# Optimization experiments

Measured on AMD Instinct MI355X. Metric: run time of the kernel, lower is better.

The kernel has to match this reference:

```python
import jax, jax.numpy as jnp
import numpy as np

SLOPE = 25.0  # fast-sigmoid surrogate slope (snntorch default)

@jax.custom_vjp
def spike(u):
    # Heaviside spike with fast-sigmoid surrogate gradient
    return (u > 0).astype(u.dtype)

def _spike_fwd(u):
    return spike(u), u

def _spike_bwd(u, g):
    return (g / (1.0 + SLOPE * jnp.abs(u)) ** 2,)

spike.defvjp(_spike_fwd, _spike_bwd)


def setup_inputs() -> dict:
    key = jax.random.key(0)
    B, N_IN, T = 256, 700, 100
    H1, H2, O = 2048, 2048, 20
    ks = jax.random.split(key, 6)

    def lin(k, out_d, in_d):
        s = 1.0 / np.sqrt(in_d)
        kw, kb = jax.random.split(k)
        W = jax.random.uniform(kw, (out_d, in_d), minval=-s, maxval=s, dtype=jnp.float32)
        b = jax.random.uniform(kb, (out_d,), minval=-s, maxval=s, dtype=jnp.float32)
        return W, b

    W1, b1 = lin(ks[0], H1, N_IN)
    W2, b2 = lin(ks[1], H2, H1)
    V, _ = lin(ks[2], H2, H2)  # learned recurrent weight of RecurrentAhpc
    W3, b3 = lin(ks[3], O, H2)
    data = jax.random.normal(ks[4], (B, N_IN, T), dtype=jnp.float32)
    f32 = lambda v: jnp.asarray(v, jnp.float32)
    return dict(
        data=data,
        W1=W1, b1=b1, W2=W2, b2=b2, V=V, W3=W3, b3=b3,
        beta1=f32(0.9), thr1=f32(1.0),
        beta_r=f32(0.9), thr_r=f32(1.0),
        back_beta=f32(0.85), alpha=f32(0.6),
        beta2=f32(0.9), thr2=f32(1.0),
    )


def _forward(data, W1, b1, W2, b2, V, W3, b3,
             beta1, thr1, beta_r, thr_r, back_beta, alpha, beta2, thr2):
    B = data.shape[0]
    H1, H2, O = W1.shape[0], W2.shape[0], W3.shape[0]
    xs = jnp.transpose(data, (2, 0, 1))  # [T, B, N_in]
    z = lambda d: jnp.zeros((B, d), dtype=data.dtype)
    init = (z(H1), z(H2), z(H2), z(H2), z(O))  # mem1, mem_r, ahp, spk_r, mem2

    def step(carry, x_t):
        mem1, mem_r, ahp, spk_r, mem2 = carry
        # layer 1: Linear + Leaky (reset-by-subtract)
        mem1 = beta1 * mem1 + x_t @ W1.T + b1
        s1 = spike(mem1 - thr1)
        mem1 = mem1 - s1 * thr1
        # layer 2: Linear + recurrent AHP leaky neuron
        cur = s1 @ W2.T + b2 + spk_r @ V.T
        mem_r = beta_r * mem_r + cur - ahp
        s_r = spike(mem_r - thr_r)
        mem_r = mem_r - s_r * thr_r
        ahp = back_beta * ahp + alpha * s_r  # after-hyperpolarization current
        # layer 3: Linear + Leaky output
        mem2 = beta2 * mem2 + s_r @ W3.T + b3
        s2 = spike(mem2 - thr2)
        mem2 = mem2 - s2 * thr2
        return (mem1, mem_r, ahp, s_r, mem2), s2

    _, spk_rec = jax.lax.scan(step, init, xs)
    return spk_rec  # [T, B, num_outputs]


def reference(data, W1, b1, W2, b2, V, W3, b3,
              beta1, thr1, beta_r, thr_r, back_beta, alpha, beta2, thr2):
    return _forward(data, W1, b1, W2, b2, V, W3, b3,
                    beta1, thr1, beta_r, thr_r, back_beta, alpha, beta2, thr2)
```

## Files before the change

kernel.cpp:

```cpp
#include <hip/hip_runtime.h>
#include <hip/hip_bf16.h>
#include <cstdint>

#define T_STEPS 100
#define BATCH 256
#define NIN 700
#define H1 2048
#define H2 2048
#define NOUT 20
#define VKS 8
#define TCHUNK 10

typedef __attribute__((ext_vector_type(8))) short bf16x8;
typedef __attribute__((ext_vector_type(4))) float f32x4;
typedef unsigned long long ull;

__device__ __forceinline__ void async16(void* lds, const void* g) {
    __builtin_amdgcn_global_load_lds(
        (const __attribute__((address_space(1))) unsigned int*)g,
        (__attribute__((address_space(3))) unsigned int*)lds, 16, 0, 0);
}

__device__ __forceinline__ unsigned short f2bf(float x) {
    __hip_bfloat16 h = __float2bfloat16(x);
    return *(unsigned short*)&h;
}
__device__ __forceinline__ float bf2f(unsigned short u) {
    __hip_bfloat16 h = *(__hip_bfloat16*)&u;
    return __bfloat162float(h);
}

__global__ __launch_bounds__(256) void split_kernel(
    const float* __restrict__ W2, const float* __restrict__ V,
    unsigned short* __restrict__ Bsplit)
{
    const size_t D = (size_t)2048 * 4096;
    size_t i = (size_t)blockIdx.x * 256 + threadIdx.x;
    int j = (int)(i >> 12), k = (int)(i & 4095);
    float w = (k < 2048) ? W2[(size_t)j * 2048 + k] : V[(size_t)j * 2048 + (k - 2048)];
    unsigned short h = f2bf(w);
    float r1 = w - bf2f(h);
    unsigned short m = f2bf(r1);
    float r2 = r1 - bf2f(m);
    unsigned short l = f2bf(r2);
    Bsplit[i] = h;
    Bsplit[D + i] = m;
    Bsplit[2 * D + i] = l;
}

__global__ __launch_bounds__(256) void w1split_kernel(
    const float* __restrict__ W1, unsigned short* __restrict__ W1f)
{
    const size_t P = (size_t)88 * 2048 * 8;
    int id = blockIdx.x * 256 + threadIdx.x;
    int g = id >> 11, j = id & 2047;
    unsigned short h8[8], m8[8], l8[8];
    #pragma unroll
    for (int e = 0; e < 8; ++e) {
        int k = g * 8 + e;
        float v = (k < NIN) ? W1[(size_t)j * NIN + k] : 0.f;
        unsigned short h = f2bf(v); float r1 = v - bf2f(h);
        unsigned short m = f2bf(r1); float r2 = r1 - bf2f(m);
        h8[e] = h; m8[e] = m; l8[e] = f2bf(r2);
    }
    size_t base = (((size_t)g * 2048) + j) * 8;
    *(uint4*)(W1f + base)         = *(uint4*)h8;
    *(uint4*)(W1f + P + base)     = *(uint4*)m8;
    *(uint4*)(W1f + 2 * P + base) = *(uint4*)l8;
}

__global__ __launch_bounds__(256) void l1m_kernel(
    const float* __restrict__ data, const unsigned short* __restrict__ W1f,
    const float* __restrict__ b1,
    const float* __restrict__ p_beta1, const float* __restrict__ p_thr1,
    ull* __restrict__ s1bits)
{
    __shared__ __align__(16) char smem[33280];
    unsigned short* Af = (unsigned short*)smem;
    const int tid = threadIdx.x, lane = tid & 63, w = tid >> 6;
    const int n16 = lane & 15, q = lane >> 4;
    const int jt = blockIdx.x & 7, b = blockIdx.x >> 3;
    const int j0w = jt * 256 + w * 64;
    const float* xb = data + (size_t)b * (NIN * T_STEPS);
    const size_t P = (size_t)88 * 2048 * 8;

    f32x4 acc[7][4] = {};
    for (int c = 0; c < 22; ++c) {
        const int kbase = c * 32;
        for (int it = tid; it < 448; it += 256) {
            int g = it / 112, t = it - g * 112;
            unsigned short h8[8], m8[8], l8[8];
            #pragma unroll
            for (int e = 0; e < 8; ++e) {
                int k = kbase + g * 8 + e;
                float v = (t < T_STEPS && k < NIN) ? xb[(size_t)k * T_STEPS + t] : 0.f;
                unsigned short h = f2bf(v); float r1 = v - bf2f(h);
                unsigned short m = f2bf(r1); float r2 = r1 - bf2f(m);
                h8[e] = h; m8[e] = m; l8[e] = f2bf(r2);
            }
            unsigned short* dst = Af + g * 896 + t * 8;
            *(uint4*)(dst)        = *(uint4*)h8;
            *(uint4*)(dst + 3584) = *(uint4*)m8;
            *(uint4*)(dst + 7168) = *(uint4*)l8;
        }
        __syncthreads();
        bf16x8 bh[4], bm[4], bl[4];
        const size_t gq = (size_t)(c * 4 + q);
        #pragma unroll
        for (int n = 0; n < 4; ++n) {
            size_t off = (gq * 2048 + (size_t)(j0w + n * 16 + n16)) * 8;
            bh[n] = *(const bf16x8*)(W1f + off);
            bm[n] = *(const bf16x8*)(W1f + P + off);
            bl[n] = *(const bf16x8*)(W1f + 2 * P + off);
        }
        #pragma unroll
        for (int m = 0; m < 7; ++m) {
            const unsigned short* ap = Af + q * 896 + (m * 16 + n16) * 8;
            bf16x8 ah = *(const bf16x8*)(ap);
            bf16x8 am = *(const bf16x8*)(ap + 3584);
            bf16x8 al = *(const bf16x8*)(ap + 7168);
            #pragma unroll
            for (int n = 0; n < 4; ++n) {
                acc[m][n] = __builtin_amdgcn_mfma_f32_16x16x32_bf16(ah, bh[n], acc[m][n], 0, 0, 0);
                acc[m][n] = __builtin_amdgcn_mfma_f32_16x16x32_bf16(ah, bm[n], acc[m][n], 0, 0, 0);
                acc[m][n] = __builtin_amdgcn_mfma_f32_16x16x32_bf16(am, bh[n], acc[m][n], 0, 0, 0);
                acc[m][n] = __builtin_amdgcn_mfma_f32_16x16x32_bf16(ah, bl[n], acc[m][n], 0, 0, 0);
                acc[m][n] = __builtin_amdgcn_mfma_f32_16x16x32_bf16(al, bh[n], acc[m][n], 0, 0, 0);
                acc[m][n] = __builtin_amdgcn_mfma_f32_16x16x32_bf16(am, bm[n], acc[m][n], 0, 0, 0);
            }
        }
        __syncthreads();
    }
    float* Cw = (float*)smem + w * (32 * 65);
    const float beta1 = *p_beta1, thr1 = *p_thr1;
    const float b1j = b1[j0w + lane];
    float mem = 0.f;
    for (int s = 0; s < 4; ++s) {
        #pragma unroll
        for (int mm = 0; mm < 2; ++mm) {
            int m = s * 2 + mm;
            if (m < 7) {
                #pragma unroll
                for (int n = 0; n < 4; ++n)
                    #pragma unroll
                    for (int r = 0; r < 4; ++r)
                        Cw[(mm * 16 + q * 4 + r) * 65 + n * 16 + n16] = acc[m][n][r];
            }
        }
        int tcnt = (s < 3) ? 32 : 4;
        for (int tt = 0; tt < tcnt; ++tt) {
            float v = Cw[tt * 65 + lane];
            mem = fmaf(beta1, mem, v) + b1j;
            bool pred = (mem - thr1) > 0.f;
            ull mask = __ballot(pred);
            if (pred) mem -= thr1;
            if (lane == 0) {
                int tg = s * 32 + tt;
                s1bits[((size_t)tg * BATCH + b) * 32 + jt * 4 + w] = mask;
            }
        }
    }
}

__global__ __launch_bounds__(256) void expand_kernel(
    const ull* __restrict__ bits_t0,
    unsigned short* __restrict__ plane)
{
    const int row = blockIdx.x;
    const int tid = threadIdx.x;
    ull word = bits_t0[(size_t)row * 32 + (tid >> 3)];
    unsigned int byte = (unsigned int)(word >> ((tid & 7) * 8)) & 0xFFu;
    unsigned short o8[8];
    #pragma unroll
    for (int e = 0; e < 8; ++e)
        o8[e] = (byte >> e) & 1u ? (unsigned short)0x3F80 : (unsigned short)0;
    *(uint4*)(plane + (size_t)row * 2048 + tid * 8) = *(uint4*)o8;
}

__global__ __launch_bounds__(256, 2) void xw2_kernel(
    const unsigned short* __restrict__ S1c,
    const unsigned short* __restrict__ Bsplit,
    float* __restrict__ X2c)
{
    __shared__ __align__(16) unsigned short Alds[128 * 64];
    __shared__ __align__(16) unsigned short Blds[3 * 64 * 64];
    const int bid = blockIdx.x;
    const int x = bid & 7;
    const int i = bid >> 3;
    const int ntl = i / 20;
    const int mt = i - ntl * 20;
    const int n0 = (x * 4 + ntl) << 6;
    const int tid = threadIdx.x, lane = tid & 63, w = tid >> 6;
    const unsigned short* Abase = S1c + ((size_t)mt << 7) * 2048;
    f32x4 acc[2][4] = {};
    for (int c = 0; c < 32; ++c) {
        const int kin = c << 6;
        #pragma unroll
        for (int ii = 0; ii < 4; ++ii) {
            int gi = (ii << 8) + tid;
            int row = gi >> 3, g8 = gi & 7;
            async16(Alds + ((size_t)gi << 3),
                    Abase + (size_t)row * 2048 + kin + ((g8 ^ (row & 7)) << 3));
        }
        #pragma unroll
        for (int term = 0; term < 3; ++term) {
            const unsigned short* Bg = Bsplit + ((size_t)term << 23);
            #pragma unroll
            for (int ii = 0; ii < 2; ++ii) {
                int d = (w << 7) + (ii << 6) + lane;
                int row = d >> 3, g8 = d & 7;
                async16(Blds + (((term << 9) + (w << 7) + (ii << 6)) << 3),
                        Bg + (size_t)(n0 + row) * 4096 + kin + ((g8 ^ (row & 7)) << 3));
            }
        }
        __syncthreads();
        #pragma unroll
        for (int kk = 0; kk < 2; ++kk) {
            const int q = lane >> 4, k16 = (kk << 2) + q;
            bf16x8 af[2];
            #pragma unroll
            for (int ii = 0; ii < 2; ++ii) {
                int ra = (w << 5) + (ii << 4) + (lane & 15);
                af[ii] = *(const bf16x8*)(Alds + (((ra << 3) + (k16 ^ (ra & 7))) << 3));
            }
            #pragma unroll
            for (int term = 0; term < 3; ++term) {
                bf16x8 bfr[4];
                #pragma unroll
                for (int j = 0; j < 4; ++j) {
                    int rb = (j << 4) + (lane & 15);
                    bfr[j] = *(const bf16x8*)(Blds +
                              (((term << 9) + (rb << 3) + (k16 ^ (rb & 7))) << 3));
                }
                #pragma unroll
                for (int ii = 0; ii < 2; ++ii)
                    #pragma unroll
                    for (int j = 0; j < 4; ++j)
                        acc[ii][j] = __builtin_amdgcn_mfma_f32_16x16x32_bf16(
                            af[ii], bfr[j], acc[ii][j], 0, 0, 0);
            }
        }
        __syncthreads();
    }
    float* Xp = X2c + ((size_t)mt << 7) * 2048;
    #pragma unroll
    for (int ii = 0; ii < 2; ++ii) {
        int rg = (w << 5) + (ii << 4) + ((lane >> 4) << 2);
        #pragma unroll
        for (int j = 0; j < 4; ++j) {
            int cg = n0 + (j << 4) + (lane & 15);
            #pragma unroll
            for (int r = 0; r < 4; ++r)
                Xp[(size_t)(rg + r) * 2048 + cg] = acc[ii][j][r];
        }
    }
}

__global__ __launch_bounds__(256, 2) void vgemm_kernel(
    const unsigned short* __restrict__ spk,
    const unsigned short* __restrict__ Bsplit,
    float* __restrict__ Cpart)
{
    __shared__ __align__(16) unsigned short Alds[256 * 64];
    __shared__ __align__(16) unsigned short Blds[3 * 64 * 64];
    const int bid = blockIdx.x;
    const int nt = bid & 31, ks = bid >> 5;
    const int n0 = nt << 6;
    const int tid = threadIdx.x, lane = tid & 63, w = tid >> 6;
    f32x4 acc[4][4] = {};
    for (int c = 0; c < 4; ++c) {
        const int kin = (ks << 8) + (c << 6);
        #pragma unroll
        for (int ii = 0; ii < 8; ++ii) {
            int gi = (ii << 8) + tid;
            int row = gi >> 3, g8 = gi & 7;
            async16(Alds + ((size_t)gi << 3),
                    spk + (size_t)row * 2048 + kin + ((g8 ^ (row & 7)) << 3));
        }
        #pragma unroll
        for (int term = 0; term < 3; ++term) {
            const unsigned short* Bg = Bsplit + ((size_t)term << 23);
            #pragma unroll
            for (int ii = 0; ii < 2; ++ii) {
                int d = (w << 7) + (ii << 6) + lane;
                int row = d >> 3, g8 = d & 7;
                async16(Blds + (((term << 9) + (w << 7) + (ii << 6)) << 3),
                        Bg + (size_t)(n0 + row) * 4096 + 2048 + kin + ((g8 ^ (row & 7)) << 3));
            }
        }
        __syncthreads();
        #pragma unroll
        for (int kk = 0; kk < 2; ++kk) {
            const int q = lane >> 4, k16 = (kk << 2) + q;
            bf16x8 af[4];
            #pragma unroll
            for (int ii = 0; ii < 4; ++ii) {
                int ra = (w << 6) + (ii << 4) + (lane & 15);
                af[ii] = *(const bf16x8*)(Alds + (((ra << 3) + (k16 ^ (ra & 7))) << 3));
            }
            #pragma unroll
            for (int term = 0; term < 3; ++term) {
                bf16x8 bfr[4];
                #pragma unroll
                for (int j = 0; j < 4; ++j) {
                    int rb = (j << 4) + (lane & 15);
                    bfr[j] = *(const bf16x8*)(Blds +
                              (((term << 9) + (rb << 3) + (k16 ^ (rb & 7))) << 3));
                }
                #pragma unroll
                for (int ii = 0; ii < 4; ++ii)
                    #pragma unroll
                    for (int j = 0; j < 4; ++j)
                        acc[ii][j] = __builtin_amdgcn_mfma_f32_16x16x32_bf16(
                            af[ii], bfr[j], acc[ii][j], 0, 0, 0);
            }
        }
        __syncthreads();
    }
    float* Cp = Cpart + ((size_t)ks << 19);
    #pragma unroll
    for (int ii = 0; ii < 4; ++ii) {
        int rg = (w << 6) + (ii << 4) + ((lane >> 4) << 2);
        #pragma unroll
        for (int j = 0; j < 4; ++j) {
            int cg = n0 + (j << 4) + (lane & 15);
            #pragma unroll
            for (int r = 0; r < 4; ++r)
                Cp[(size_t)(rg + r) * 2048 + cg] = acc[ii][j][r];
        }
    }
}

__global__ __launch_bounds__(256) void l2fin_kernel(
    const float* __restrict__ Cpart, const float* __restrict__ X2t,
    const float* __restrict__ b2,
    float* __restrict__ mem_r, float* __restrict__ ahp,
    unsigned short* __restrict__ spk_out,
    ull* __restrict__ srbits_t,
    const float* __restrict__ p_beta_r, const float* __restrict__ p_thr_r,
    const float* __restrict__ p_back_beta, const float* __restrict__ p_alpha)
{
    const int b = blockIdx.x, t = threadIdx.x;
    const int lane = t & 63, wv = t >> 6;
    const float beta_r = *p_beta_r, thr_r = *p_thr_r;
    const float bb = *p_back_beta, al = *p_alpha;
    #pragma unroll
    for (int u = 0; u < 8; ++u) {
        int j = t + (u << 8);
        size_t cidx = (size_t)b * 2048 + j;
        float x = 0.f;
        #pragma unroll
        for (int p = 0; p < VKS; ++p) x += Cpart[((size_t)p << 19) + cidx];
        float cur = x + X2t[cidx] + b2[j];
        float m = fmaf(beta_r, mem_r[cidx], cur) - ahp[cidx];
        bool pred = (m - thr_r) > 0.f;
        ull mask = __ballot(pred);
        float s = pred ? 1.f : 0.f;
        if (pred) m -= thr_r;
        mem_r[cidx] = m;
        ahp[cidx] = fmaf(bb, ahp[cidx], al * s);
        spk_out[cidx] = pred ? (unsigned short)0x3F80 : (unsigned short)0;
        if (lane == 0) srbits_t[((size_t)b << 5) + (u << 2) + wv] = mask;
    }
}

__global__ __launch_bounds__(256) void w3out_kernel(
    const ull* __restrict__ srbits, const float* __restrict__ W3,
    const float* __restrict__ b3, float* __restrict__ out,
    const float* __restrict__ p_beta2, const float* __restrict__ p_thr2)
{
    __shared__ ull bitsLDS[T_STEPS * 32];
    __shared__ float red[4][10];
    const int b = blockIdx.x, tid = threadIdx.x, lane = tid & 63, wv = tid >> 6;
    for (int i = tid; i < T_STEPS * 32; i += 256)
        bitsLDS[i] = srbits[((size_t)(i >> 5) * BATCH + b) * 32 + (i & 31)];
    __syncthreads();
    const float beta2 = *p_beta2, thr2 = *p_thr2;
    for (int pass = 0; pass < 2; ++pass) {
        float w8[10][8];
        #pragma unroll
        for (int o = 0; o < 10; ++o) {
            const float4* wp = (const float4*)(W3 + (size_t)(pass * 10 + o) * 2048 + tid * 8);
            float4 a = wp[0], c = wp[1];
            w8[o][0] = a.x; w8[o][1] = a.y; w8[o][2] = a.z; w8[o][3] = a.w;
            w8[o][4] = c.x; w8[o][5] = c.y; w8[o][6] = c.z; w8[o][7] = c.w;
        }
        float m2 = 0.f;
        for (int t = 0; t < T_STEPS; ++t) {
            ull word = bitsLDS[(t << 5) + (tid >> 3)];
            unsigned int byte = (unsigned int)(word >> ((tid & 7) * 8)) & 0xFFu;
            float po[10];
            #pragma unroll
            for (int o = 0; o < 10; ++o) {
                float v = 0.f;
                #pragma unroll
                for (int e = 0; e < 8; ++e)
                    v += ((byte >> e) & 1u) ? w8[o][e] : 0.f;
                #pragma unroll
                for (int msk = 32; msk > 0; msk >>= 1)
                    v += __shfl_xor(v, msk, 64);
                po[o] = v;
            }
            if (lane == 0) {
                #pragma unroll
                for (int o = 0; o < 10; ++o) red[wv][o] = po[o];
            }
            __syncthreads();
            if (tid < 10) {
                float cur = red[0][tid] + red[1][tid] + red[2][tid] + red[3][tid]
                          + b3[pass * 10 + tid];
                float m = fmaf(beta2, m2, cur);
                bool pred = (m - thr2) > 0.f;
                float s2 = pred ? 1.f : 0.f;
                if (pred) m -= thr2;
                m2 = m;
                out[((size_t)t * BATCH + b) * NOUT + pass * 10 + tid] = s2;
            }
            __syncthreads();
        }
    }
}

extern "C" void kernel_launch(void* const* d_in, const int* in_sizes, int n_in,
                              void* d_out, int out_size, void* d_ws, size_t ws_size,
                              hipStream_t stream)
{
    const float* data   = (const float*)d_in[0];
    const float* W1     = (const float*)d_in[1];
    const float* b1     = (const float*)d_in[2];
    const float* W2     = (const float*)d_in[3];
    const float* b2     = (const float*)d_in[4];
    const float* V      = (const float*)d_in[5];
    const float* W3     = (const float*)d_in[6];
    const float* b3     = (const float*)d_in[7];
    const float* beta1  = (const float*)d_in[8];
    const float* thr1   = (const float*)d_in[9];
    const float* beta_r = (const float*)d_in[10];
    const float* thr_r  = (const float*)d_in[11];
    const float* back_beta = (const float*)d_in[12];
    const float* alpha  = (const float*)d_in[13];
    const float* beta2  = (const float*)d_in[14];
    const float* thr2   = (const float*)d_in[15];
    float* out = (float*)d_out;
    (void)in_sizes; (void)n_in; (void)out_size; (void)ws_size;

    char* p = (char*)d_ws;
    auto carve = [&](size_t bytes) {
        char* r = p; p += (bytes + 255) & ~(size_t)255; return r;
    };
    ull* s1bits = (ull*)carve((size_t)T_STEPS*BATCH*32*8);
    ull* srbits = (ull*)carve((size_t)T_STEPS*BATCH*32*8);
    unsigned short* spk0 = (unsigned short*)carve((size_t)BATCH*H2*2);
    unsigned short* spk1 = (unsigned short*)carve((size_t)BATCH*H2*2);
    float* mem_r = (float*)carve((size_t)BATCH*H2*4);
    float* ahp   = (float*)carve((size_t)BATCH*H2*4);
    unsigned short* Bsplit = (unsigned short*)carve((size_t)3*2048*4096*2);
    char* uni = carve((size_t)VKS*BATCH*H2*4);
    unsigned short* S1c = (unsigned short*)uni;
    float* Cpart = (float*)uni;
    float* X2c = (float*)carve((size_t)TCHUNK*BATCH*H2*4);
    unsigned short* W1f = (unsigned short*)carve((size_t)3*88*2048*8*2);

    hipMemsetAsync(spk0, 0, (size_t)BATCH*H2*2, stream);
    hipMemsetAsync(mem_r, 0, (size_t)BATCH*H2*4, stream);
    hipMemsetAsync(ahp,  0, (size_t)BATCH*H2*4, stream);

    split_kernel<<<(2048*4096)/256, 256, 0, stream>>>(W2, V, Bsplit);
    w1split_kernel<<<704, 256, 0, stream>>>(W1, W1f);
    l1m_kernel<<<2048, 256, 0, stream>>>(data, W1f, b1, beta1, thr1, s1bits);

    unsigned short* spk[2] = {spk0, spk1};
    for (int ck = 0; ck < T_STEPS / TCHUNK; ++ck) {
        const int t0 = ck * TCHUNK;
        expand_kernel<<<TCHUNK*BATCH, 256, 0, stream>>>(
            s1bits + (size_t)t0*BATCH*32, S1c);
        xw2_kernel<<<8*4*2*TCHUNK, 256, 0, stream>>>(S1c, Bsplit, X2c);
        for (int tt = 0; tt < TCHUNK; ++tt) {
            const int t = t0 + tt;
            vgemm_kernel<<<256, 256, 0, stream>>>(spk[t & 1], Bsplit, Cpart);
            l2fin_kernel<<<256, 256, 0, stream>>>(Cpart,
                                                  X2c + (size_t)tt*BATCH*H2, b2,
                                                  mem_r, ahp, spk[(t + 1) & 1],
                                                  srbits + (size_t)t*BATCH*32,
                                                  beta_r, thr_r, back_beta, alpha);
        }
    }
    w3out_kernel<<<256, 256, 0, stream>>>(srbits, W3, b3, out, beta2, thr2);
}
```

Measured before the change: 3.642 ms.

## Fuse recurrent GEMM and layer-2 neuron update via per-column-tile spin barrier

Merges the split-K recurrent GEMM and the layer-2 finalize kernel into one launch per timestep. Each block writes its partial tile, then the 8 split-K blocks that share a column tile synchronise through a monotonically increasing atomic counter. After that barrier each block reduces and applies the neuron update for its own 32 rows by 64 columns. This removes one kernel launch per step and the gap between the two kernels. It relies on all 256 blocks being co-resident to avoid deadlock and adds spin-wait and fence overhead.

```diff
diff --git a/kernel.cpp b/kernel.cpp
--- a/kernel.cpp
+++ b/kernel.cpp
@@ -256,10 +256,17 @@
     }
 }
 
-__global__ __launch_bounds__(256, 2) void vgemm_kernel(
+__global__ __launch_bounds__(256, 2) void vstep_kernel(
     const unsigned short* __restrict__ spk,
     const unsigned short* __restrict__ Bsplit,
-    float* __restrict__ Cpart)
+    float* __restrict__ Cpart,
+    const float* __restrict__ X2t, const float* __restrict__ b2,
+    float* __restrict__ mem_r, float* __restrict__ ahp,
+    unsigned short* __restrict__ spk_out,
+    ull* __restrict__ srbits_t,
+    unsigned int* __restrict__ done, unsigned int expected,
+    const float* __restrict__ p_beta_r, const float* __restrict__ p_thr_r,
+    const float* __restrict__ p_back_beta, const float* __restrict__ p_alpha)
 {
     __shared__ __align__(16) unsigned short Alds[256 * 64];
     __shared__ __align__(16) unsigned short Blds[3 * 64 * 64];
@@ -317,41 +324,41 @@
         }
         __syncthreads();
     }
-    float* Cp = Cpart + ((size_t)ks << 19);
-    #pragma unroll
-    for (int ii = 0; ii < 4; ++ii) {
-        int rg = (w << 6) + (ii << 4) + ((lane >> 4) << 2);
-        #pragma unroll
-        for (int j = 0; j < 4; ++j) {
-            int cg = n0 + (j << 4) + (lane & 15);
-            #pragma unroll
-            for (int r = 0; r < 4; ++r)
-                Cp[(size_t)(rg + r) * 2048 + cg] = acc[ii][j][r];
-        }
-    }
-}
-
-__global__ __launch_bounds__(256) void l2fin_kernel(
-    const float* __restrict__ Cpart, const float* __restrict__ X2t,
-    const float* __restrict__ b2,
-    float* __restrict__ mem_r, float* __restrict__ ahp,
-    unsigned short* __restrict__ spk_out,
-    ull* __restrict__ srbits_t,
-    const float* __restrict__ p_beta_r, const float* __restrict__ p_thr_r,
-    const float* __restrict__ p_back_beta, const float* __restrict__ p_alpha)
-{
-    const int b = blockIdx.x, t = threadIdx.x;
-    const int lane = t & 63, wv = t >> 6;
+    {
+        float* Cp = Cpart + ((size_t)ks << 19);
+        #pragma unroll
+        for (int ii = 0; ii < 4; ++ii) {
+            int rg = (w << 6) + (ii << 4) + ((lane >> 4) << 2);
+            #pragma unroll
+            for (int j = 0; j < 4; ++j) {
+                int cg = n0 + (j << 4) + (lane & 15);
+                #pragma unroll
+                for (int r = 0; r < 4; ++r)
+                    Cp[(size_t)(rg + r) * 2048 + cg] = acc[ii][j][r];
+            }
+        }
+    }
+    __syncthreads();
+    if (tid == 0) {
+        __threadfence();
+        atomicAdd(&done[nt], 1u);
+        while (atomicAdd(&done[nt], 0u) < expected)
+            __builtin_amdgcn_s_sleep(2);
+    }
+    __syncthreads();
+    __threadfence();
     const float beta_r = *p_beta_r, thr_r = *p_thr_r;
     const float bb = *p_back_beta, al = *p_alpha;
+    const int jj = n0 + lane;
+    const float b2j = b2[jj];
     #pragma unroll
     for (int u = 0; u < 8; ++u) {
-        int j = t + (u << 8);
-        size_t cidx = (size_t)b * 2048 + j;
+        int b = (ks << 5) + (w << 3) + u;
+        size_t cidx = ((size_t)b << 11) + jj;
         float x = 0.f;
         #pragma unroll
         for (int p = 0; p < VKS; ++p) x += Cpart[((size_t)p << 19) + cidx];
-        float cur = x + X2t[cidx] + b2[j];
+        float cur = x + X2t[cidx] + b2j;
         float m = fmaf(beta_r, mem_r[cidx], cur) - ahp[cidx];
         bool pred = (m - thr_r) > 0.f;
         ull mask = __ballot(pred);
@@ -360,7 +367,7 @@
         mem_r[cidx] = m;
         ahp[cidx] = fmaf(bb, ahp[cidx], al * s);
         spk_out[cidx] = pred ? (unsigned short)0x3F80 : (unsigned short)0;
-        if (lane == 0) srbits_t[((size_t)b << 5) + (u << 2) + wv] = mask;
+        if (lane == 0) srbits_t[((size_t)b << 5) + nt] = mask;
     }
 }
 
@@ -454,6 +461,7 @@
     unsigned short* spk1 = (unsigned short*)carve((size_t)BATCH*H2*2);
     float* mem_r = (float*)carve((size_t)BATCH*H2*4);
     float* ahp   = (float*)carve((size_t)BATCH*H2*4);
+    unsigned int* done = (unsigned int*)carve(32 * sizeof(unsigned int));
     unsigned short* Bsplit = (unsigned short*)carve((size_t)3*2048*4096*2);
     char* uni = carve((size_t)VKS*BATCH*H2*4);
     unsigned short* S1c = (unsigned short*)uni;
@@ -464,6 +472,7 @@
     hipMemsetAsync(spk0, 0, (size_t)BATCH*H2*2, stream);
     hipMemsetAsync(mem_r, 0, (size_t)BATCH*H2*4, stream);
     hipMemsetAsync(ahp,  0, (size_t)BATCH*H2*4, stream);
+    hipMemsetAsync(done, 0, 32 * sizeof(unsigned int), stream);
 
     split_kernel<<<(2048*4096)/256, 256, 0, stream>>>(W2, V, Bsplit);
     w1split_kernel<<<704, 256, 0, stream>>>(W1, W1f);
@@ -477,12 +486,11 @@
         xw2_kernel<<<8*4*2*TCHUNK, 256, 0, stream>>>(S1c, Bsplit, X2c);
         for (int tt = 0; tt < TCHUNK; ++tt) {
             const int t = t0 + tt;
-            vgemm_kernel<<<256, 256, 0, stream>>>(spk[t & 1], Bsplit, Cpart);
-            l2fin_kernel<<<256, 256, 0, stream>>>(Cpart,
-                                                  X2c + (size_t)tt*BATCH*H2, b2,
-                                                  mem_r, ahp, spk[(t + 1) & 1],
-                                                  srbits + (size_t)t*BATCH*32,
-                                                  beta_r, thr_r, back_beta, alpha);
+            vstep_kernel<<<256, 256, 0, stream>>>(
+                spk[t & 1], Bsplit, Cpart, X2c + (size_t)tt*BATCH*H2, b2,
+                mem_r, ahp, spk[(t + 1) & 1], srbits + (size_t)t*BATCH*32,
+                done, 8u*(unsigned)(t + 1),
+                beta_r, thr_r, back_beta, alpha);
         }
     }
     w3out_kernel<<<256, 256, 0, stream>>>(srbits, W3, b3, out, beta2, thr2);
```

After: 7.025 ms. +92.9%, slower.

## Expand spike bitmasks to bf16 inside GEMM kernels instead of materialising planes

Applied to the files above, without the earlier changes.

The expand kernel and the bf16 spike planes are removed. xw2 and vgemm now read packed 64-bit spike masks and expand them to bf16 1.0/0.0 values directly into swizzled LDS. l2fin writes only bitmasks into one (T+1)-plane bitmask buffer, with plane 0 zeroed as the initial state. This cuts global traffic and one launch per chunk, but replaces async global-to-LDS copies for the A operand with synchronous register-computed LDS stores.

```diff
diff --git a/kernel.cpp b/kernel.cpp
--- a/kernel.cpp
+++ b/kernel.cpp
@@ -28,6 +28,15 @@
 __device__ __forceinline__ float bf2f(unsigned short u) {
     __hip_bfloat16 h = *(__hip_bfloat16*)&u;
     return __bfloat162float(h);
+}
+
+__device__ __forceinline__ void byte_to_u4(unsigned int byte, unsigned int* u) {
+    #pragma unroll
+    for (int p = 0; p < 4; ++p) {
+        int bit = p << 1;
+        u[p] = (((byte >> bit) & 1u) ? 0x3F80u : 0u)
+             | (((byte >> (bit + 1)) & 1u) ? 0x3F800000u : 0u);
+    }
 }
 
 __global__ __launch_bounds__(256) void split_kernel(
@@ -162,23 +171,8 @@
     }
 }
 
-__global__ __launch_bounds__(256) void expand_kernel(
-    const ull* __restrict__ bits_t0,
-    unsigned short* __restrict__ plane)
-{
-    const int row = blockIdx.x;
-    const int tid = threadIdx.x;
-    ull word = bits_t0[(size_t)row * 32 + (tid >> 3)];
-    unsigned int byte = (unsigned int)(word >> ((tid & 7) * 8)) & 0xFFu;
-    unsigned short o8[8];
-    #pragma unroll
-    for (int e = 0; e < 8; ++e)
-        o8[e] = (byte >> e) & 1u ? (unsigned short)0x3F80 : (unsigned short)0;
-    *(uint4*)(plane + (size_t)row * 2048 + tid * 8) = *(uint4*)o8;
-}
-
 __global__ __launch_bounds__(256, 2) void xw2_kernel(
-    const unsigned short* __restrict__ S1c,
+    const ull* __restrict__ bits0,
     const unsigned short* __restrict__ Bsplit,
     float* __restrict__ X2c)
 {
@@ -191,16 +185,21 @@
     const int mt = i - ntl * 20;
     const int n0 = (x * 4 + ntl) << 6;
     const int tid = threadIdx.x, lane = tid & 63, w = tid >> 6;
-    const unsigned short* Abase = S1c + ((size_t)mt << 7) * 2048;
+    const int ar = tid >> 1, ah2 = tid & 1;
     f32x4 acc[2][4] = {};
     for (int c = 0; c < 32; ++c) {
         const int kin = c << 6;
-        #pragma unroll
-        for (int ii = 0; ii < 4; ++ii) {
-            int gi = (ii << 8) + tid;
-            int row = gi >> 3, g8 = gi & 7;
-            async16(Alds + ((size_t)gi << 3),
-                    Abase + (size_t)row * 2048 + kin + ((g8 ^ (row & 7)) << 3));
+        {
+            ull word = bits0[(size_t)(mt * 128 + ar) * 32 + c];
+            unsigned int half = (unsigned int)(word >> (ah2 * 32));
+            #pragma unroll
+            for (int gi2 = 0; gi2 < 4; ++gi2) {
+                int g = (ah2 << 2) + gi2;
+                unsigned int u[4];
+                byte_to_u4((half >> (gi2 * 8)) & 0xFFu, u);
+                int slot = (ar << 3) + (g ^ (ar & 7));
+                *(uint4*)(Alds + (slot << 3)) = *(uint4*)u;
+            }
         }
         #pragma unroll
         for (int term = 0; term < 3; ++term) {
@@ -257,7 +256,7 @@
 }
 
 __global__ __launch_bounds__(256, 2) void vgemm_kernel(
-    const unsigned short* __restrict__ spk,
+    const ull* __restrict__ srb_in,
     const unsigned short* __restrict__ Bsplit,
     float* __restrict__ Cpart)
 {
@@ -270,12 +269,15 @@
     f32x4 acc[4][4] = {};
     for (int c = 0; c < 4; ++c) {
         const int kin = (ks << 8) + (c << 6);
-        #pragma unroll
-        for (int ii = 0; ii < 8; ++ii) {
-            int gi = (ii << 8) + tid;
-            int row = gi >> 3, g8 = gi & 7;
-            async16(Alds + ((size_t)gi << 3),
-                    spk + (size_t)row * 2048 + kin + ((g8 ^ (row & 7)) << 3));
+        {
+            ull word = srb_in[((size_t)tid << 5) + (ks << 2) + c];
+            #pragma unroll
+            for (int g8 = 0; g8 < 8; ++g8) {
+                unsigned int u[4];
+                byte_to_u4((unsigned int)(word >> (g8 << 3)) & 0xFFu, u);
+                int gdst = (tid << 3) + (g8 ^ (tid & 7));
+                *(uint4*)(Alds + (gdst << 3)) = *(uint4*)u;
+            }
         }
         #pragma unroll
         for (int term = 0; term < 3; ++term) {
@@ -335,8 +337,7 @@
     const float* __restrict__ Cpart, const float* __restrict__ X2t,
     const float* __restrict__ b2,
     float* __restrict__ mem_r, float* __restrict__ ahp,
-    unsigned short* __restrict__ spk_out,
-    ull* __restrict__ srbits_t,
+    ull* __restrict__ srbits_out,
     const float* __restrict__ p_beta_r, const float* __restrict__ p_thr_r,
     const float* __restrict__ p_back_beta, const float* __restrict__ p_alpha)
 {
@@ -359,8 +360,7 @@
         if (pred) m -= thr_r;
         mem_r[cidx] = m;
         ahp[cidx] = fmaf(bb, ahp[cidx], al * s);
-        spk_out[cidx] = pred ? (unsigned short)0x3F80 : (unsigned short)0;
-        if (lane == 0) srbits_t[((size_t)b << 5) + (u << 2) + wv] = mask;
+        if (lane == 0) srbits_out[((size_t)b << 5) + (u << 2) + wv] = mask;
     }
 }
 
@@ -444,24 +444,22 @@
     float* out = (float*)d_out;
     (void)in_sizes; (void)n_in; (void)out_size; (void)ws_size;
 
+    const size_t PLANE = (size_t)BATCH * 32;
+
     char* p = (char*)d_ws;
     auto carve = [&](size_t bytes) {
         char* r = p; p += (bytes + 255) & ~(size_t)255; return r;
     };
     ull* s1bits = (ull*)carve((size_t)T_STEPS*BATCH*32*8);
-    ull* srbits = (ull*)carve((size_t)T_STEPS*BATCH*32*8);
-    unsigned short* spk0 = (unsigned short*)carve((size_t)BATCH*H2*2);
-    unsigned short* spk1 = (unsigned short*)carve((size_t)BATCH*H2*2);
+    ull* srbAll = (ull*)carve((size_t)(T_STEPS+1)*BATCH*32*8);
     float* mem_r = (float*)carve((size_t)BATCH*H2*4);
     float* ahp   = (float*)carve((size_t)BATCH*H2*4);
     unsigned short* Bsplit = (unsigned short*)carve((size_t)3*2048*4096*2);
-    char* uni = carve((size_t)VKS*BATCH*H2*4);
-    unsigned short* S1c = (unsigned short*)uni;
-    float* Cpart = (float*)uni;
+    float* Cpart = (float*)carve((size_t)VKS*BATCH*H2*4);
     float* X2c = (float*)carve((size_t)TCHUNK*BATCH*H2*4);
     unsigned short* W1f = (unsigned short*)carve((size_t)3*88*2048*8*2);
 
-    hipMemsetAsync(spk0, 0, (size_t)BATCH*H2*2, stream);
+    hipMemsetAsync(srbAll, 0, PLANE*8, stream);
     hipMemsetAsync(mem_r, 0, (size_t)BATCH*H2*4, stream);
     hipMemsetAsync(ahp,  0, (size_t)BATCH*H2*4, stream);
 
@@ -469,21 +467,21 @@
     w1split_kernel<<<704, 256, 0, stream>>>(W1, W1f);
     l1m_kernel<<<2048, 256, 0, stream>>>(data, W1f, b1, beta1, thr1, s1bits);
 
-    unsigned short* spk[2] = {spk0, spk1};
     for (int ck = 0; ck < T_STEPS / TCHUNK; ++ck) {
         const int t0 = ck * TCHUNK;
-        expand_kernel<<<TCHUNK*BATCH, 256, 0, stream>>>(
-            s1bits + (size_t)t0*BATCH*32, S1c);
-        xw2_kernel<<<8*4*2*TCHUNK, 256, 0, stream>>>(S1c, Bsplit, X2c);
+        xw2_kernel<<<640, 256, 0, stream>>>(s1bits + (size_t)t0*BATCH*32,
+                                            Bsplit, X2c);
         for (int tt = 0; tt < TCHUNK; ++tt) {
             const int t = t0 + tt;
-            vgemm_kernel<<<256, 256, 0, stream>>>(spk[t & 1], Bsplit, Cpart);
+            vgemm_kernel<<<256, 256, 0, stream>>>(srbAll + (size_t)t*PLANE,
+                                                  Bsplit, Cpart);
             l2fin_kernel<<<256, 256, 0, stream>>>(Cpart,
                                                   X2c + (size_t)tt*BATCH*H2, b2,
-                                                  mem_r, ahp, spk[(t + 1) & 1],
-                                                  srbits + (size_t)t*BATCH*32,
+                                                  mem_r, ahp,
+                                                  srbAll + (size_t)(t+1)*PLANE,
                                                   beta_r, thr_r, back_beta, alpha);
         }
     }
-    w3out_kernel<<<256, 256, 0, stream>>>(srbits, W3, b3, out, beta2, thr2);
-}
+    w3out_kernel<<<256, 256, 0, stream>>>(srbAll + PLANE, W3, b3, out,
+                                          beta2, thr2);
+}
```

New measurement: 3.764 ms. +3.4%, slower.
